# Performance work log

Measured on AMD Instinct MI355X. Metric: run time of the kernel, lower is better.

## Reference

```python
import jax, jax.numpy as jnp
import numpy as np
from jax import lax

N = 1024
N_I = 64
N_AV = 10
ALPHA = 0.5
RHO = 0.9
GAMMA = 1.0


def _make_params(seed=0):
    rng = np.random.RandomState(seed)
    diluition = 1.0 - N_AV / N
    W = rng.uniform(-1, 1, [N, N])
    W = W * (rng.uniform(0, 1, [N, N]) > diluition)
    eig = np.linalg.eigvals(W)
    W = (RHO * W / np.max(np.absolute(eig))).astype(np.float32)
    # N_i != 1 branch: gaussian input weights scaled by gamma
    W_in = (GAMMA * rng.randn(N_I, N)).astype(np.float32)
    return jnp.asarray(W), jnp.asarray(W_in)


def setup_inputs() -> dict:
    key = jax.random.key(0)
    Input = jax.random.normal(key, (128, N_I, 512), dtype=jnp.float32)
    W, W_in = _make_params()
    return {"Input": Input, "W": W, "W_in": W_in}


def reference(Input, W, W_in):
    # Input: [B, N_i, T] -> X: [B, N, T]
    B = Input.shape[0]
    x0 = jnp.zeros((B, W.shape[0]), dtype=Input.dtype)
    seq = jnp.transpose(Input, (2, 0, 1))  # [T, B, N_i]

    def step(x, s):
        x = (1.0 - ALPHA) * x + ALPHA * jnp.tanh(s @ W_in + x @ W)
        return x, x

    _, X = lax.scan(step, x0, seq)  # [T, B, N]
    return jnp.transpose(X, (1, 2, 0))  # [B, N, T]
```

## Files before the change

### kernel.cpp

```cpp
#include <hip/hip_runtime.h>
#include <hip/hip_fp16.h>
#include <cstdint>
#include <cstddef>

#define BB 128
#define NN 1024
#define NI 64
#define TT 512
#define MAXNNZ 16384
#define NE 28
#define TH 16

#define WS_OFFS   0u
#define WS_IDX    16384u
#define WS_VAL    65536u
#define WS_PERM   131072u
#define WS_IPERM  135168u
#define WS_XSTATE 139264u
#define WS_WINP   663552u
#define WS_EIDX2  925696u
#define WS_CNT16  983040u
#define WS_OFF16  1048576u
#define WS_U      1114112u

__global__ __launch_bounds__(64) void k_count16(const float* __restrict__ W, int* __restrict__ cnt16) {
    int bc = blockIdx.x;
    int s = bc & 15, g = bc >> 4;
    int col = g * 64 + threadIdx.x;
    int c = 0;
    for (int q = 0; q < 64; ++q) {
        int k = s * 64 + q;
        c += (W[(size_t)k * NN + col] != 0.0f) ? 1 : 0;
    }
    cnt16[col * 16 + s] = c;
}

__global__ __launch_bounds__(1024) void k_scan3(const int* __restrict__ cnt16, int* __restrict__ offs,
                                                int* __restrict__ off16) {
    __shared__ int s[NN];
    int tid = threadIdx.x;
    int t = 0;
#pragma unroll
    for (int q = 0; q < 16; ++q) t += cnt16[tid * 16 + q];
    s[tid] = t;
    __syncthreads();
    for (int d = 1; d < NN; d <<= 1) {
        int v = (tid >= d) ? s[tid - d] : 0;
        __syncthreads();
        s[tid] += v;
        __syncthreads();
    }
    int incl = s[tid];
    offs[tid + 1] = (incl < MAXNNZ) ? incl : MAXNNZ;
    if (tid == 0) offs[0] = 0;
    int base = incl - t;
#pragma unroll
    for (int q = 0; q < 16; ++q) {
        off16[tid * 16 + q] = base;
        base += cnt16[tid * 16 + q];
    }
}

__global__ __launch_bounds__(64) void k_fill16(const float* __restrict__ W, const int* __restrict__ off16,
                                               unsigned short* __restrict__ idx, float* __restrict__ val) {
    int bc = blockIdx.x;
    int s = bc & 15, g = bc >> 4;
    int col = g * 64 + threadIdx.x;
    int p = off16[col * 16 + s];
    for (int q = 0; q < 64; ++q) {
        int k = s * 64 + q;
        float w = W[(size_t)k * NN + col];
        if (w != 0.0f) { idx[p] = (unsigned short)k; val[p] = w; ++p; }
    }
}

__global__ __launch_bounds__(1024) void k_rankchoice(const int* __restrict__ offs,
        const unsigned short* __restrict__ gidx, int* __restrict__ perm, int* __restrict__ iperm,
        unsigned short* __restrict__ eidx2) {
    __shared__ int sc[NN];
    __shared__ unsigned short rk[NN][NE];
    __shared__ unsigned short scnt[NN];
    __shared__ unsigned char ctr8[448][2][32];
    int n = threadIdx.x;
    sc[n] = offs[n + 1] - offs[n];
    __syncthreads();
    int myc = sc[n];
    int r = 0;
    for (int m = 0; m < NN; ++m) {
        int cm = sc[m];
        r += (cm > myc || (cm == myc && m < n)) ? 1 : 0;
    }
    perm[r] = n;
    iperm[n] = r;
    __syncthreads();
    {
        int rr = n;
        int c = perm[rr];
        int o0 = offs[c];
        int cn = offs[c + 1] - o0;
        if (cn > NE) cn = NE;
        scnt[rr] = (unsigned short)cn;
        for (int j = 0; j < cn; ++j) rk[rr][j] = (unsigned short)iperm[(int)gidx[o0 + j]];
    }
    __syncthreads();
    int tid = n;
    if (tid < 448) {
        int w = tid / NE, j = tid % NE;
        for (int h = 0; h < 2; ++h) {
            unsigned char* mc = &ctr8[tid][h][0];
            for (int b = 0; b < 32; ++b) mc[b] = 0;
            unsigned sel = 0u;
            for (int l = 0; l < 32; ++l) {
                int rr = 64 * w + 32 * h + l;
                if (j < (int)scnt[rr]) {
                    int rv = (int)rk[rr][j];
                    int bA = rv & 31, bB = (rv ^ (rv >> 5)) & 31;
                    if (mc[bA] <= mc[bB]) mc[bA]++;
                    else { sel |= (1u << l); mc[bB]++; }
                }
            }
            for (int sweep = 0; sweep < 12; ++sweep) {
                bool ch = false;
                for (int l = 0; l < 32; ++l) {
                    int rr = 64 * w + 32 * h + l;
                    if (j < (int)scnt[rr]) {
                        int rv = (int)rk[rr][j];
                        int bA = rv & 31, bB = (rv ^ (rv >> 5)) & 31;
                        int isB = (int)((sel >> l) & 1u);
                        int cur = isB ? bB : bA, alt = isB ? bA : bB;
                        if ((int)mc[cur] > (int)mc[alt] + 1) {
                            mc[cur]--; mc[alt]++;
                            sel ^= (1u << l);
                            ch = true;
                        }
                    }
                }
                if (!ch) break;
            }
            for (int l = 0; l < 32; ++l) {
                int rr = 64 * w + 32 * h + l;
                if (j < (int)scnt[rr]) {
                    int rv = (int)rk[rr][j];
                    int bB = (rv ^ (rv >> 5)) & 31;
                    int addr = ((sel >> l) & 1u) ? (4096 + (((rv & ~31) | bB) << 2))
                                                 : (rv << 2);
                    eidx2[j * NN + rr] = (unsigned short)addr;
                }
            }
            int minb = 0, minl = (int)mc[0];
            for (int b = 1; b < 32; ++b)
                if ((int)mc[b] < minl) { minl = (int)mc[b]; minb = b; }
            unsigned short pad = (unsigned short)(minb << 2);
            for (int l = 0; l < 32; ++l) {
                int rr = 64 * w + 32 * h + l;
                if (j >= (int)scnt[rr]) eidx2[j * NN + rr] = pad;
            }
        }
    }
}

__global__ __launch_bounds__(256) void k_permwin(const float* __restrict__ Win, const int* __restrict__ perm,
                                                 float* __restrict__ Winp) {
    int idx = blockIdx.x * 256 + threadIdx.x;
    int i = idx >> 10, r = idx & 1023;
    Winp[idx] = Win[(i << 10) + perm[r]];
}

__global__ __launch_bounds__(256) void k_uproj3(const float* __restrict__ In, const float* __restrict__ Winp,
                                                __half* __restrict__ U, int t0c, int nblk) {
    int b  = blockIdx.x / nblk;
    int tq = blockIdx.x % nblk;
    int t0 = t0c + tq * 32;
    __shared__ float s[NI][36];
    int tid = threadIdx.x;
    {
        int i = tid >> 2, g = tid & 3;
        const float* ip = In + ((size_t)b * NI + i) * TT + t0 + g * 8;
        float4 v0 = *(const float4*)(ip);
        float4 v1 = *(const float4*)(ip + 4);
        *(float4*)&s[i][g * 8]     = v0;
        *(float4*)&s[i][g * 8 + 4] = v1;
    }
    __syncthreads();
    const float4* W4 = (const float4*)Winp;
    uint2* U2 = (uint2*)U;
    for (int th = 0; th < 2; ++th) {
        float4 acc[16];
#pragma unroll
        for (int t = 0; t < 16; ++t) acc[t] = make_float4(0.f, 0.f, 0.f, 0.f);
        for (int i = 0; i < NI; ++i) {
            float4 w = W4[(size_t)i * 256 + tid];
            float4 s0 = *(const float4*)&s[i][th * 16];
            float4 s1 = *(const float4*)&s[i][th * 16 + 4];
            float4 s2 = *(const float4*)&s[i][th * 16 + 8];
            float4 s3 = *(const float4*)&s[i][th * 16 + 12];
            const float sv[16] = {s0.x, s0.y, s0.z, s0.w, s1.x, s1.y, s1.z, s1.w,
                                  s2.x, s2.y, s2.z, s2.w, s3.x, s3.y, s3.z, s3.w};
#pragma unroll
            for (int t = 0; t < 16; ++t) {
                acc[t].x = fmaf(w.x, sv[t], acc[t].x);
                acc[t].y = fmaf(w.y, sv[t], acc[t].y);
                acc[t].z = fmaf(w.z, sv[t], acc[t].z);
                acc[t].w = fmaf(w.w, sv[t], acc[t].w);
            }
        }
#pragma unroll
        for (int t = 0; t < 16; ++t) {
            __half2 h01 = __floats2half2_rn(acc[t].x, acc[t].y);
            __half2 h23 = __floats2half2_rn(acc[t].z, acc[t].w);
            uint2 pk;
            pk.x = *(unsigned int*)&h01;
            pk.y = *(unsigned int*)&h23;
            U2[((size_t)(tq * 32 + th * 16 + t) * BB + b) * 256 + tid] = pk;
        }
    }
}

__device__ __forceinline__ float fast_tanh(float z) {
    float a = fabsf(z) * 2.885390082f;
    a = fminf(a, 60.0f);
    float e = __builtin_amdgcn_exp2f(a);
    float r = 1.0f - __fdividef(2.0f, e + 1.0f);
    return z < 0.0f ? -r : r;
}

#define L28(M) \
  M(0) M(1) M(2) M(3) M(4) M(5) M(6) M(7) M(8) M(9) M(10) M(11) M(12) M(13) \
  M(14) M(15) M(16) M(17) M(18) M(19) M(20) M(21) M(22) M(23) M(24) M(25) M(26) M(27)

#define DW(i)  float w##i; int a##i;
#define IW(i)  { a##i = (int)eidx2[(i) * NN + n]; \
                 w##i = (cnt > i) ? gval[o0 + i] : 0.0f; }

#define PIN_ALL \
  asm volatile("" : "+v"(w0),"+v"(w1),"+v"(w2),"+v"(w3),"+v"(w4),"+v"(w5),"+v"(w6),"+v"(w7)); \
  asm volatile("" : "+v"(w8),"+v"(w9),"+v"(w10),"+v"(w11),"+v"(w12),"+v"(w13),"+v"(w14),"+v"(w15)); \
  asm volatile("" : "+v"(w16),"+v"(w17),"+v"(w18),"+v"(w19),"+v"(w20),"+v"(w21),"+v"(w22),"+v"(w23)); \
  asm volatile("" : "+v"(w24),"+v"(w25),"+v"(w26),"+v"(w27)); \
  asm volatile("" : "+v"(a0),"+v"(a1),"+v"(a2),"+v"(a3),"+v"(a4),"+v"(a5),"+v"(a6),"+v"(a7)); \
  asm volatile("" : "+v"(a8),"+v"(a9),"+v"(a10),"+v"(a11),"+v"(a12),"+v"(a13),"+v"(a14),"+v"(a15)); \
  asm volatile("" : "+v"(a16),"+v"(a17),"+v"(a18),"+v"(a19),"+v"(a20),"+v"(a21),"+v"(a22),"+v"(a23)); \
  asm volatile("" : "+v"(a24),"+v"(a25),"+v"(a26),"+v"(a27));

#define GRP(J, i0, i1, i2, i3) \
  if ((J) < wmax) { \
    float q0 = *(const float*)(xp + a##i0); \
    float q1 = *(const float*)(xp + a##i1); \
    float q2 = *(const float*)(xp + a##i2); \
    float q3 = *(const float*)(xp + a##i3); \
    z0 = fmaf(w##i0, q0, z0); z1 = fmaf(w##i1, q1, z1); \
    z2 = fmaf(w##i2, q2, z2); z3 = fmaf(w##i3, q3, z3); \
  }

#define GATHER_ALL \
  GRP(0, 0,1,2,3)      GRP(4, 4,5,6,7)      GRP(8, 8,9,10,11) \
  GRP(12, 12,13,14,15) GRP(16, 16,17,18,19) GRP(20, 20,21,22,23) \
  GRP(24, 24,25,26,27)

#define STEP(PH, XDST) { \
    float u = unx; \
    int tn = t + 1; tn = (tn < Tc) ? tn : (Tc - 1); \
    unx = (float)Ub[(size_t)tn * ustep]; \
    const char* xp = xb + (PH); \
    float z0 = u, z1 = 0.f, z2 = 0.f, z3 = 0.f; \
    GATHER_ALL \
    x = 0.5f * x + 0.5f * fast_tanh((z0 + z1) + (z2 + z3)); \
    XDST = x; \
    float* wb = (float*)(xb + ((PH) ^ 8192)); \
    wb[n] = x; \
    wb[NN + nB] = x; \
    __syncthreads(); \
    ++t; \
}

__global__ __launch_bounds__(1024, 4)
void k_step(const __half* __restrict__ U,
            const int* __restrict__ offs, const unsigned short* __restrict__ eidx2,
            const float* __restrict__ gval, const int* __restrict__ perm,
            float* __restrict__ out, float* __restrict__ xstate, int t0, int Tc) {
    __shared__ float xbuf[2][2][NN];
    int b = blockIdx.x, n = threadIdx.x;
    int c = perm[n];
    int nB = (n & ~31) | ((n ^ (n >> 5)) & 31);

    int o0 = offs[c];
    int cnt = offs[c + 1] - o0;
    L28(DW)
    L28(IW)
    PIN_ALL

    int wmax = cnt;
#pragma unroll
    for (int d = 1; d < 64; d <<= 1) {
        int o = __shfl_xor(wmax, d);
        wmax = wmax > o ? wmax : o;
    }
    wmax = __builtin_amdgcn_readfirstlane(wmax);

    float x = (t0 == 0) ? 0.0f : xstate[((size_t)b << 10) + n];
    xbuf[0][0][n] = x;
    xbuf[0][1][nB] = x;
    __syncthreads();

    char* xb = (char*)&xbuf[0][0][0];
    const __half* Ub = U + (size_t)b * NN + n;
    const size_t ustep = (size_t)BB * NN;
    float unx = (float)Ub[0];

    for (int tb = 0; tb < Tc; tb += TH) {
        PIN_ALL
        int t = tb;
        float y0, y1, y2, y3, y4, y5, y6, y7, y8, y9, y10, y11, y12, y13, y14, y15;
        STEP(0,    y0)
        STEP(8192, y1)
        STEP(0,    y2)
        STEP(8192, y3)
        STEP(0,    y4)
        STEP(8192, y5)
        STEP(0,    y6)
        STEP(8192, y7)
        STEP(0,    y8)
        STEP(8192, y9)
        STEP(0,    y10)
        STEP(8192, y11)
        STEP(0,    y12)
        STEP(8192, y13)
        STEP(0,    y14)
        STEP(8192, y15)
        float4* op = (float4*)(out + ((size_t)b * NN + c) * TT + (size_t)(t0 + tb));
        op[0] = make_float4(y0,  y1,  y2,  y3);
        op[1] = make_float4(y4,  y5,  y6,  y7);
        op[2] = make_float4(y8,  y9,  y10, y11);
        op[3] = make_float4(y12, y13, y14, y15);
    }
    if (Tc < TT) xstate[((size_t)b << 10) + n] = x;
}

extern "C" void kernel_launch(void* const* d_in, const int* in_sizes, int n_in,
                              void* d_out, int out_size, void* d_ws, size_t ws_size,
                              hipStream_t stream) {
    const float* In  = (const float*)d_in[0];
    const float* W   = (const float*)d_in[1];
    const float* Win = (const float*)d_in[2];
    float* out = (float*)d_out;
    char* ws = (char*)d_ws;
    int* offs           = (int*)(ws + WS_OFFS);
    unsigned short* idx = (unsigned short*)(ws + WS_IDX);
    float* val          = (float*)(ws + WS_VAL);
    int* perm           = (int*)(ws + WS_PERM);
    int* iperm          = (int*)(ws + WS_IPERM);
    float* xstate       = (float*)(ws + WS_XSTATE);
    float* Winp         = (float*)(ws + WS_WINP);
    unsigned short* eidx2 = (unsigned short*)(ws + WS_EIDX2);
    int* cnt16          = (int*)(ws + WS_CNT16);
    int* off16          = (int*)(ws + WS_OFF16);
    __half* U           = (__half*)(ws + WS_U);

    int Tc = 32;
    const int cands[5] = {512, 256, 128, 64, 32};
    for (int i = 0; i < 5; ++i) {
        if ((size_t)WS_U + (size_t)cands[i] * BB * NN * 2 <= ws_size) { Tc = cands[i]; break; }
    }

    k_count16<<<256, 64, 0, stream>>>(W, cnt16);
    k_scan3<<<1, 1024, 0, stream>>>(cnt16, offs, off16);
    k_fill16<<<256, 64, 0, stream>>>(W, off16, idx, val);
    k_rankchoice<<<1, 1024, 0, stream>>>(offs, idx, perm, iperm, eidx2);
    k_permwin<<<256, 256, 0, stream>>>(Win, perm, Winp);

    for (int t0 = 0; t0 < TT; t0 += Tc) {
        int nblk = Tc / 32;
        k_uproj3<<<BB * nblk, 256, 0, stream>>>(In, Winp, U, t0, nblk);
        k_step<<<BB, 1024, 0, stream>>>(U, offs, eidx2, val, perm, out, xstate, t0, Tc);
    }
}
```

Measured before the change: 667.7 us.

## Overlap next-chunk input projection with recurrence via extra blocks in fused kernel

```diff
diff --git a/kernel.cpp b/kernel.cpp
--- a/kernel.cpp
+++ b/kernel.cpp
@@ -10,6 +10,7 @@
 #define MAXNNZ 16384
 #define NE 28
 #define TH 16
+#define TCC 256
 
 #define WS_OFFS   0u
 #define WS_IDX    16384u
@@ -22,6 +23,7 @@
 #define WS_CNT16  983040u
 #define WS_OFF16  1048576u
 #define WS_U      1114112u
+#define WS_U2     (WS_U + 67108864u)
 
 __global__ __launch_bounds__(64) void k_count16(const float* __restrict__ W, int* __restrict__ cnt16) {
     int bc = blockIdx.x;
@@ -80,7 +82,7 @@
     __shared__ int sc[NN];
     __shared__ unsigned short rk[NN][NE];
     __shared__ unsigned short scnt[NN];
-    __shared__ unsigned char ctr8[448][2][32];
+    __shared__ unsigned char ctr8[896][32];
     int n = threadIdx.x;
     sc[n] = offs[n + 1] - offs[n];
     __syncthreads();
@@ -104,57 +106,56 @@
     }
     __syncthreads();
     int tid = n;
-    if (tid < 448) {
-        int w = tid / NE, j = tid % NE;
-        for (int h = 0; h < 2; ++h) {
-            unsigned char* mc = &ctr8[tid][h][0];
-            for (int b = 0; b < 32; ++b) mc[b] = 0;
-            unsigned sel = 0u;
+    if (tid < 896) {
+        int task = tid >> 1, h = tid & 1;
+        int w = task / NE, j = task % NE;
+        unsigned char* mc = &ctr8[tid][0];
+        for (int b = 0; b < 32; ++b) mc[b] = 0;
+        unsigned sel = 0u;
+        for (int l = 0; l < 32; ++l) {
+            int rr = 64 * w + 32 * h + l;
+            if (j < (int)scnt[rr]) {
+                int rv = (int)rk[rr][j];
+                int bA = rv & 31, bB = (rv ^ (rv >> 5)) & 31;
+                if (mc[bA] <= mc[bB]) mc[bA]++;
+                else { sel |= (1u << l); mc[bB]++; }
+            }
+        }
+        for (int sweep = 0; sweep < 12; ++sweep) {
+            bool ch = false;
             for (int l = 0; l < 32; ++l) {
                 int rr = 64 * w + 32 * h + l;
                 if (j < (int)scnt[rr]) {
                     int rv = (int)rk[rr][j];
                     int bA = rv & 31, bB = (rv ^ (rv >> 5)) & 31;
-                    if (mc[bA] <= mc[bB]) mc[bA]++;
-                    else { sel |= (1u << l); mc[bB]++; }
-                }
-            }
-            for (int sweep = 0; sweep < 12; ++sweep) {
-                bool ch = false;
-                for (int l = 0; l < 32; ++l) {
-                    int rr = 64 * w + 32 * h + l;
-                    if (j < (int)scnt[rr]) {
-                        int rv = (int)rk[rr][j];
-                        int bA = rv & 31, bB = (rv ^ (rv >> 5)) & 31;
-                        int isB = (int)((sel >> l) & 1u);
-                        int cur = isB ? bB : bA, alt = isB ? bA : bB;
-                        if ((int)mc[cur] > (int)mc[alt] + 1) {
-                            mc[cur]--; mc[alt]++;
-                            sel ^= (1u << l);
-                            ch = true;
-                        }
+                    int isB = (int)((sel >> l) & 1u);
+                    int cur = isB ? bB : bA, alt = isB ? bA : bB;
+                    if ((int)mc[cur] > (int)mc[alt] + 1) {
+                        mc[cur]--; mc[alt]++;
+                        sel ^= (1u << l);
+                        ch = true;
                     }
                 }
-                if (!ch) break;
-            }
-            for (int l = 0; l < 32; ++l) {
-                int rr = 64 * w + 32 * h + l;
-                if (j < (int)scnt[rr]) {
-                    int rv = (int)rk[rr][j];
-                    int bB = (rv ^ (rv >> 5)) & 31;
-                    int addr = ((sel >> l) & 1u) ? (4096 + (((rv & ~31) | bB) << 2))
-                                                 : (rv << 2);
-                    eidx2[j * NN + rr] = (unsigned short)addr;
-                }
-            }
-            int minb = 0, minl = (int)mc[0];
-            for (int b = 1; b < 32; ++b)
-                if ((int)mc[b] < minl) { minl = (int)mc[b]; minb = b; }
-            unsigned short pad = (unsigned short)(minb << 2);
-            for (int l = 0; l < 32; ++l) {
-                int rr = 64 * w + 32 * h + l;
-                if (j >= (int)scnt[rr]) eidx2[j * NN + rr] = pad;
-            }
+            }
+            if (!ch) break;
+        }
+        for (int l = 0; l < 32; ++l) {
+            int rr = 64 * w + 32 * h + l;
+            if (j < (int)scnt[rr]) {
+                int rv = (int)rk[rr][j];
+                int bB = (rv ^ (rv >> 5)) & 31;
+                int addr = ((sel >> l) & 1u) ? (4096 + (((rv & ~31) | bB) << 2))
+                                             : (rv << 2);
+                eidx2[j * NN + rr] = (unsigned short)addr;
+            }
+        }
+        int minb = 0, minl = (int)mc[0];
+        for (int b = 1; b < 32; ++b)
+            if ((int)mc[b] < minl) { minl = (int)mc[b]; minb = b; }
+        unsigned short pad = (unsigned short)(minb << 2);
+        for (int l = 0; l < 32; ++l) {
+            int rr = 64 * w + 32 * h + l;
+            if (j >= (int)scnt[rr]) eidx2[j * NN + rr] = pad;
         }
     }
 }
@@ -171,15 +172,17 @@
     int b  = blockIdx.x / nblk;
     int tq = blockIdx.x % nblk;
     int t0 = t0c + tq * 32;
-    __shared__ float s[NI][36];
+    __shared__ float s[32][NI + 1];
     int tid = threadIdx.x;
     {
         int i = tid >> 2, g = tid & 3;
         const float* ip = In + ((size_t)b * NI + i) * TT + t0 + g * 8;
         float4 v0 = *(const float4*)(ip);
         float4 v1 = *(const float4*)(ip + 4);
-        *(float4*)&s[i][g * 8]     = v0;
-        *(float4*)&s[i][g * 8 + 4] = v1;
+        s[g * 8 + 0][i] = v0.x; s[g * 8 + 1][i] = v0.y;
+        s[g * 8 + 2][i] = v0.z; s[g * 8 + 3][i] = v0.w;
+        s[g * 8 + 4][i] = v1.x; s[g * 8 + 5][i] = v1.y;
+        s[g * 8 + 6][i] = v1.z; s[g * 8 + 7][i] = v1.w;
     }
     __syncthreads();
     const float4* W4 = (const float4*)Winp;
@@ -190,18 +193,13 @@
         for (int t = 0; t < 16; ++t) acc[t] = make_float4(0.f, 0.f, 0.f, 0.f);
         for (int i = 0; i < NI; ++i) {
             float4 w = W4[(size_t)i * 256 + tid];
-            float4 s0 = *(const float4*)&s[i][th * 16];
-            float4 s1 = *(const float4*)&s[i][th * 16 + 4];
-            float4 s2 = *(const float4*)&s[i][th * 16 + 8];
-            float4 s3 = *(const float4*)&s[i][th * 16 + 12];
-            const float sv[16] = {s0.x, s0.y, s0.z, s0.w, s1.x, s1.y, s1.z, s1.w,
-                                  s2.x, s2.y, s2.z, s2.w, s3.x, s3.y, s3.z, s3.w};
 #pragma unroll
             for (int t = 0; t < 16; ++t) {
-                acc[t].x = fmaf(w.x, sv[t], acc[t].x);
-                acc[t].y = fmaf(w.y, sv[t], acc[t].y);
-                acc[t].z = fmaf(w.z, sv[t], acc[t].z);
-                acc[t].w = fmaf(w.w, sv[t], acc[t].w);
+                float sv = s[th * 16 + t][i];
+                acc[t].x = fmaf(w.x, sv, acc[t].x);
+                acc[t].y = fmaf(w.y, sv, acc[t].y);
+                acc[t].z = fmaf(w.z, sv, acc[t].z);
+                acc[t].w = fmaf(w.w, sv, acc[t].w);
             }
         }
 #pragma unroll
@@ -274,66 +272,117 @@
 }
 
 __global__ __launch_bounds__(1024, 4)
-void k_step(const __half* __restrict__ U,
-            const int* __restrict__ offs, const unsigned short* __restrict__ eidx2,
-            const float* __restrict__ gval, const int* __restrict__ perm,
-            float* __restrict__ out, float* __restrict__ xstate, int t0, int Tc) {
-    __shared__ float xbuf[2][2][NN];
-    int b = blockIdx.x, n = threadIdx.x;
-    int c = perm[n];
-    int nB = (n & ~31) | ((n ^ (n >> 5)) & 31);
-
-    int o0 = offs[c];
-    int cnt = offs[c + 1] - o0;
-    L28(DW)
-    L28(IW)
-    PIN_ALL
-
-    int wmax = cnt;
-#pragma unroll
-    for (int d = 1; d < 64; d <<= 1) {
-        int o = __shfl_xor(wmax, d);
-        wmax = wmax > o ? wmax : o;
-    }
-    wmax = __builtin_amdgcn_readfirstlane(wmax);
-
-    float x = (t0 == 0) ? 0.0f : xstate[((size_t)b << 10) + n];
-    xbuf[0][0][n] = x;
-    xbuf[0][1][nB] = x;
-    __syncthreads();
-
-    char* xb = (char*)&xbuf[0][0][0];
-    const __half* Ub = U + (size_t)b * NN + n;
-    const size_t ustep = (size_t)BB * NN;
-    float unx = (float)Ub[0];
-
-    for (int tb = 0; tb < Tc; tb += TH) {
+void k_fused(const __half* __restrict__ Uread, __half* __restrict__ Uwrite,
+             const float* __restrict__ In, const float* __restrict__ Winp,
+             const int* __restrict__ offs, const unsigned short* __restrict__ eidx2,
+             const float* __restrict__ gval, const int* __restrict__ perm,
+             float* __restrict__ out, float* __restrict__ xstate,
+             int t0, int Tc) {
+    __shared__ float smem[4 * 32 * 65];
+    int tid = threadIdx.x;
+    if (blockIdx.x < BB) {
+        int b = blockIdx.x, n = tid;
+        int c = perm[n];
+        int nB = (n & ~31) | ((n ^ (n >> 5)) & 31);
+        int o0 = offs[c];
+        int cnt = offs[c + 1] - o0;
+        L28(DW)
+        L28(IW)
         PIN_ALL
-        int t = tb;
-        float y0, y1, y2, y3, y4, y5, y6, y7, y8, y9, y10, y11, y12, y13, y14, y15;
-        STEP(0,    y0)
-        STEP(8192, y1)
-        STEP(0,    y2)
-        STEP(8192, y3)
-        STEP(0,    y4)
-        STEP(8192, y5)
-        STEP(0,    y6)
-        STEP(8192, y7)
-        STEP(0,    y8)
-        STEP(8192, y9)
-        STEP(0,    y10)
-        STEP(8192, y11)
-        STEP(0,    y12)
-        STEP(8192, y13)
-        STEP(0,    y14)
-        STEP(8192, y15)
-        float4* op = (float4*)(out + ((size_t)b * NN + c) * TT + (size_t)(t0 + tb));
-        op[0] = make_float4(y0,  y1,  y2,  y3);
-        op[1] = make_float4(y4,  y5,  y6,  y7);
-        op[2] = make_float4(y8,  y9,  y10, y11);
-        op[3] = make_float4(y12, y13, y14, y15);
-    }
-    if (Tc < TT) xstate[((size_t)b << 10) + n] = x;
+        int wmax = cnt;
+#pragma unroll
+        for (int d = 1; d < 64; d <<= 1) {
+            int o = __shfl_xor(wmax, d);
+            wmax = wmax > o ? wmax : o;
+        }
+        wmax = __builtin_amdgcn_readfirstlane(wmax);
+
+        float x = (t0 == 0) ? 0.0f : xstate[((size_t)b << 10) + n];
+        smem[n] = x;
+        smem[NN + nB] = x;
+        __syncthreads();
+
+        char* xb = (char*)&smem[0];
+        const __half* Ub = Uread + (size_t)b * NN + n;
+        const size_t ustep = (size_t)BB * NN;
+        float unx = (float)Ub[0];
+
+        for (int tb = 0; tb < Tc; tb += TH) {
+            PIN_ALL
+            int t = tb;
+            float y0, y1, y2, y3, y4, y5, y6, y7, y8, y9, y10, y11, y12, y13, y14, y15;
+            STEP(0,    y0)
+            STEP(8192, y1)
+            STEP(0,    y2)
+            STEP(8192, y3)
+            STEP(0,    y4)
+            STEP(8192, y5)
+            STEP(0,    y6)
+            STEP(8192, y7)
+            STEP(0,    y8)
+            STEP(8192, y9)
+            STEP(0,    y10)
+            STEP(8192, y11)
+            STEP(0,    y12)
+            STEP(8192, y13)
+            STEP(0,    y14)
+            STEP(8192, y15)
+            float4* op = (float4*)(out + ((size_t)b * NN + c) * TT + (size_t)(t0 + tb));
+            op[0] = make_float4(y0,  y1,  y2,  y3);
+            op[1] = make_float4(y4,  y5,  y6,  y7);
+            op[2] = make_float4(y8,  y9,  y10, y11);
+            op[3] = make_float4(y12, y13, y14, y15);
+        }
+        if (Tc < TT) xstate[((size_t)b << 10) + n] = x;
+    } else {
+        if (t0 + Tc >= TT) return;
+        int b = blockIdx.x - BB;
+        int sub = tid >> 8, stid = tid & 255;
+        float* sg = smem + sub * 32 * 65;
+        const float4* W4 = (const float4*)Winp;
+        uint2* U2w = (uint2*)Uwrite;
+        for (int rep = 0; rep < 2; ++rep) {
+            int tq = sub * 2 + rep;
+            int tg = t0 + Tc + tq * 32;
+            __syncthreads();
+            {
+                int i = stid >> 2, g4 = stid & 3;
+                const float* ip = In + ((size_t)b * NI + i) * TT + tg + g4 * 8;
+                float4 v0 = *(const float4*)(ip);
+                float4 v1 = *(const float4*)(ip + 4);
+                sg[(g4 * 8 + 0) * 65 + i] = v0.x; sg[(g4 * 8 + 1) * 65 + i] = v0.y;
+                sg[(g4 * 8 + 2) * 65 + i] = v0.z; sg[(g4 * 8 + 3) * 65 + i] = v0.w;
+                sg[(g4 * 8 + 4) * 65 + i] = v1.x; sg[(g4 * 8 + 5) * 65 + i] = v1.y;
+                sg[(g4 * 8 + 6) * 65 + i] = v1.z; sg[(g4 * 8 + 7) * 65 + i] = v1.w;
+            }
+            __syncthreads();
+            for (int th = 0; th < 2; ++th) {
+                float4 acc[16];
+#pragma unroll
+                for (int t = 0; t < 16; ++t) acc[t] = make_float4(0.f, 0.f, 0.f, 0.f);
+                for (int i = 0; i < NI; ++i) {
+                    float4 w = W4[(size_t)i * 256 + stid];
+#pragma unroll
+                    for (int t = 0; t < 16; ++t) {
+                        float sv = sg[(th * 16 + t) * 65 + i];
+                        acc[t].x = fmaf(w.x, sv, acc[t].x);
+                        acc[t].y = fmaf(w.y, sv, acc[t].y);
+                        acc[t].z = fmaf(w.z, sv, acc[t].z);
+                        acc[t].w = fmaf(w.w, sv, acc[t].w);
+                    }
+                }
+#pragma unroll
+                for (int t = 0; t < 16; ++t) {
+                    __half2 h01 = __floats2half2_rn(acc[t].x, acc[t].y);
+                    __half2 h23 = __floats2half2_rn(acc[t].z, acc[t].w);
+                    uint2 pk;
+                    pk.x = *(unsigned int*)&h01;
+                    pk.y = *(unsigned int*)&h23;
+                    U2w[((size_t)(tq * 32 + th * 16 + t) * BB + b) * 256 + stid] = pk;
+                }
+            }
+        }
+    }
 }
 
 extern "C" void kernel_launch(void* const* d_in, const int* in_sizes, int n_in,
@@ -354,13 +403,8 @@
     unsigned short* eidx2 = (unsigned short*)(ws + WS_EIDX2);
     int* cnt16          = (int*)(ws + WS_CNT16);
     int* off16          = (int*)(ws + WS_OFF16);
-    __half* U           = (__half*)(ws + WS_U);
-
-    int Tc = 32;
-    const int cands[5] = {512, 256, 128, 64, 32};
-    for (int i = 0; i < 5; ++i) {
-        if ((size_t)WS_U + (size_t)cands[i] * BB * NN * 2 <= ws_size) { Tc = cands[i]; break; }
-    }
+    __half* U0          = (__half*)(ws + WS_U);
+    __half* U1          = (__half*)(ws + WS_U2);
 
     k_count16<<<256, 64, 0, stream>>>(W, cnt16);
     k_scan3<<<1, 1024, 0, stream>>>(cnt16, offs, off16);
@@ -368,9 +412,17 @@
     k_rankchoice<<<1, 1024, 0, stream>>>(offs, idx, perm, iperm, eidx2);
     k_permwin<<<256, 256, 0, stream>>>(Win, perm, Winp);
 
-    for (int t0 = 0; t0 < TT; t0 += Tc) {
-        int nblk = Tc / 32;
-        k_uproj3<<<BB * nblk, 256, 0, stream>>>(In, Winp, U, t0, nblk);
-        k_step<<<BB, 1024, 0, stream>>>(U, offs, eidx2, val, perm, out, xstate, t0, Tc);
-    }
-}
+    if ((size_t)WS_U2 + (size_t)TCC * BB * NN * 2 <= ws_size) {
+        k_uproj3<<<BB * (TCC / 32), 256, 0, stream>>>(In, Winp, U0, 0, TCC / 32);
+        k_fused<<<2 * BB, 1024, 0, stream>>>(U0, U1, In, Winp, offs, eidx2, val, perm,
+                                             out, xstate, 0, TCC);
+        k_fused<<<2 * BB, 1024, 0, stream>>>(U1, U0, In, Winp, offs, eidx2, val, perm,
+                                             out, xstate, TCC, TCC);
+    } else {
+        for (int t0 = 0; t0 < TT; t0 += TCC) {
+            k_uproj3<<<BB * (TCC / 32), 256, 0, stream>>>(In, Winp, U0, t0, TCC / 32);
+            k_fused<<<BB, 1024, 0, stream>>>(U0, U0, In, Winp, offs, eidx2, val, perm,
+                                             out, xstate, t0, TT + TCC );
+        }
+    }
+}
```

Result: faster. 587.5 us (-12.0%).
